# Performance work log

Hardware: AMD Instinct MI355X
Metric: run time of the kernel (lower is better)

## Reference

```python
import jax, jax.numpy as jnp
import numpy as np

IN_DIM = 768   # 256 + 256 + 128 + 128
OUT_DIM = 256
N_EDGES = 320000
N_GRAPHS = 64


def setup_inputs() -> dict:
    key = jax.random.key(0)
    ks = jax.random.split(key, 7)
    src = jax.random.normal(ks[0], (N_EDGES, 256), dtype=jnp.float32)
    dest = jax.random.normal(ks[1], (N_EDGES, 256), dtype=jnp.float32)
    edge_attr = jax.random.normal(ks[2], (N_EDGES, 128), dtype=jnp.float32)
    u = jax.random.normal(ks[3], (N_GRAPHS, 128), dtype=jnp.float32)
    batch = jnp.sort(jax.random.randint(ks[4], (N_EDGES,), 0, N_GRAPHS, dtype=jnp.int64)) if jax.config.read('jax_enable_x64') else jnp.sort(jax.random.randint(ks[4], (N_EDGES,), 0, N_GRAPHS)).astype(jnp.int32)
    # Linear(in_dim, out_dim): torch default init ~ U(-1/sqrt(in), 1/sqrt(in))
    bound = 1.0 / np.sqrt(IN_DIM)
    W = jax.random.uniform(ks[5], (IN_DIM, OUT_DIM), dtype=jnp.float32, minval=-bound, maxval=bound)
    b = jax.random.uniform(ks[6], (OUT_DIM,), dtype=jnp.float32, minval=-bound, maxval=bound)
    return {"src": src, "dest": dest, "edge_attr": edge_attr, "u": u, "batch": batch, "W": W, "b": b}


def reference(src, dest, edge_attr, u, batch, W, b):
    # u_expanded = u[batch]; concat [dest, src, edge_attr, u_exp]; Linear + ReLU
    u_exp = jnp.take(u, batch, axis=0)                    # [E, 128]
    combined = jnp.concatenate([dest, src, edge_attr, u_exp], axis=1)  # [E, 768]
    out = combined @ W + b                                # [E, 256]
    return jax.nn.relu(out)
```

## Files before the change

### kernel.cpp

```cpp
#include <hip/hip_runtime.h>
#include <cstdint>
#include <cstddef>

#define BM 64
#define BN 256
#define BK 32
#define NT 24
#define THREADS 512
#define A_BYTES (BM * BK * 2)
#define B_BYTES (BN * BK * 2)
#define BUF_BYTES (A_BYTES + B_BYTES)
#define NBUF 3

typedef __attribute__((ext_vector_type(4))) float f32x4;
typedef __attribute__((ext_vector_type(8))) short bf16x8;
typedef __attribute__((ext_vector_type(2))) unsigned int u32x2;

__device__ __forceinline__ unsigned int f2bf(float f) {
  union { float f; uint32_t u; } v; v.f = f;
  uint32_t r = v.u + 0x7FFFu + ((v.u >> 16) & 1u);
  return r >> 16;
}

__global__ void wt_kernel(const float* __restrict__ W, unsigned short* __restrict__ WtS) {
  const int gid = blockIdx.x * 256 + threadIdx.x;
  const int kt = gid >> 10;
  const int c  = gid & 1023;
  const int n  = ((c >> 6) << 4) | (c & 15);
  const int k0 = kt * 32 + ((c >> 4) & 3) * 8;
  unsigned int p[4];
#pragma unroll
  for (int i = 0; i < 4; ++i)
    p[i] = f2bf(W[(size_t)(k0 + 2 * i) * 256 + n]) |
           (f2bf(W[(size_t)(k0 + 2 * i + 1) * 256 + n]) << 16);
  *(u32x2*)((char*)WtS + (size_t)gid * 16)     = u32x2{p[0], p[1]};
  *(u32x2*)((char*)WtS + (size_t)gid * 16 + 8) = u32x2{p[2], p[3]};
}

__global__ __launch_bounds__(THREADS, 4) void edge_gemm(
    const float* __restrict__ srcf, const float* __restrict__ destf,
    const float* __restrict__ eaf, const float* __restrict__ uf,
    const int* __restrict__ batch, const unsigned short* __restrict__ WtS,
    const float* __restrict__ bias, float* __restrict__ out)
{
  __shared__ char smem[NBUF * BUF_BYTES];
  const int tid  = threadIdx.x;
  const int lane = tid & 63;
  const int w    = tid >> 6;
  const int wr   = w >> 2;
  const int wc   = w & 3;
  const int m0   = blockIdx.x * BM;
  const int l15  = lane & 15;
  const int l4   = lane >> 4;

  const int s_row  = ((tid >> 7) << 4) | ((tid >> 1) & 15);
  const int s_coff = (((tid >> 5) & 3) << 3) | ((tid & 1) << 2);
  const int s_ae   = m0 + s_row;
  const int s_ub   = batch[s_ae];

  float bs[4];
#pragma unroll
  for (int nf = 0; nf < 4; ++nf) bs[nf] = bias[wc * 64 + nf * 16 + l15];

  f32x4 acc[2][4];
  f32x4 z = {0.f, 0.f, 0.f, 0.f};
#pragma unroll
  for (int i = 0; i < 2; ++i)
#pragma unroll
    for (int j = 0; j < 4; ++j) acc[i][j] = z;

  auto a_ptr = [&](int kt) -> const float* {
    if (kt < 8)  return destf + (size_t)s_ae * 256 + kt * 32 + s_coff;
    if (kt < 16) return srcf  + (size_t)s_ae * 256 + (kt - 8) * 32 + s_coff;
    if (kt < 20) return eaf   + (size_t)s_ae * 128 + (kt - 16) * 32 + s_coff;
    return uf + (size_t)s_ub * 128 + (kt - 20) * 32 + s_coff;
  };

  f32x4 va[2];

  auto stage = [&](int kt) {
    char* Bb = smem + (kt % NBUF) * BUF_BYTES + A_BYTES;
    const char* wb = (const char*)WtS + (size_t)kt * B_BYTES;
#pragma unroll
    for (int j = 0; j < 2; ++j) {
      const char* g = wb + (size_t)(j * 512 + tid) * 16;
      char* l = Bb + (size_t)(j * 512 + w * 64) * 16;
      __builtin_amdgcn_global_load_lds(
          (const __attribute__((address_space(1))) uint32_t*)g,
          (__attribute__((address_space(3))) uint32_t*)l, 16, 0, 0);
    }
    va[kt & 1] = *(const f32x4*)a_ptr(kt);
  };
  auto write_a = [&](int kt) {
    char* Ab = smem + (kt % NBUF) * BUF_BYTES;
    f32x4 v = va[kt & 1];
    u32x2 p;
    p[0] = f2bf(v[0]) | (f2bf(v[1]) << 16);
    p[1] = f2bf(v[2]) | (f2bf(v[3]) << 16);
    *(u32x2*)(Ab + tid * 8) = p;
  };
  auto compute = [&](int kt) {
    const char* Ab = smem + (kt % NBUF) * BUF_BYTES;
    const char* Bb = Ab + A_BYTES;
    bf16x8 af[2], bfr[4];
#pragma unroll
    for (int mf = 0; mf < 2; ++mf)
      af[mf] = *(const bf16x8*)(Ab + (((wr * 2 + mf) * 64) + l4 * 16 + l15) * 16);
#pragma unroll
    for (int nf = 0; nf < 4; ++nf)
      bfr[nf] = *(const bf16x8*)(Bb + (((wc * 4 + nf) * 64) + l4 * 16 + l15) * 16);
#pragma unroll
    for (int mf = 0; mf < 2; ++mf)
#pragma unroll
      for (int nf = 0; nf < 4; ++nf)
        acc[mf][nf] = __builtin_amdgcn_mfma_f32_16x16x32_bf16(
            af[mf], bfr[nf], acc[mf][nf], 0, 0, 0);
  };

#define STEP_SYNC()                                          \
  asm volatile("s_waitcnt vmcnt(3)" ::: "memory");           \
  __builtin_amdgcn_sched_barrier(0);                         \
  asm volatile("s_waitcnt lgkmcnt(0)" ::: "memory");         \
  __builtin_amdgcn_sched_barrier(0);                         \
  __builtin_amdgcn_s_barrier()

  stage(0);
  __builtin_amdgcn_sched_barrier(0);
  stage(1);
  __builtin_amdgcn_sched_barrier(0);
  write_a(0);
  STEP_SYNC();

#pragma unroll
  for (int kt = 0; kt < NT; ++kt) {
    if (kt + 2 < NT) stage(kt + 2);
    __builtin_amdgcn_sched_barrier(0);
    compute(kt);
    if (kt + 1 < NT) {
      write_a(kt + 1);
      STEP_SYNC();
    }
  }

#pragma unroll
  for (int mf = 0; mf < 2; ++mf) {
    const int r0 = m0 + wr * 32 + mf * 16 + l4 * 4;
#pragma unroll
    for (int nf = 0; nf < 4; ++nf) {
      const int cn = wc * 64 + nf * 16 + l15;
      const f32x4 v = acc[mf][nf];
#pragma unroll
      for (int j = 0; j < 4; ++j) {
        const float x = v[j] + bs[nf];
        out[(size_t)(r0 + j) * 256 + cn] = x > 0.f ? x : 0.f;
      }
    }
  }
#undef STEP_SYNC
}

extern "C" void kernel_launch(void* const* d_in, const int* in_sizes, int n_in,
                              void* d_out, int out_size, void* d_ws, size_t ws_size,
                              hipStream_t stream) {
  const float* srcf  = (const float*)d_in[0];
  const float* destf = (const float*)d_in[1];
  const float* eaf   = (const float*)d_in[2];
  const float* uf    = (const float*)d_in[3];
  const int*   batch = (const int*)d_in[4];
  const float* W     = (const float*)d_in[5];
  const float* bias  = (const float*)d_in[6];
  float* out = (float*)d_out;
  unsigned short* WtS = (unsigned short*)d_ws;

  wt_kernel<<<96, 256, 0, stream>>>(W, WtS);

  edge_gemm<<<320000 / BM, THREADS, 0, stream>>>(
      srcf, destf, eaf, uf, batch, WtS, bias, out);
}
```

Baseline: 282.0 us.

## Stage A in 256-wide swizzled LDS slabs and read W directly from global

Replaces the per-32-K-step pipeline, which staged A and W tiles through LDS with a barrier every step, by three large stages of 256 K columns each. Every stage loads a full 64x256 A slab as coalesced row-wise loads into double-buffered, XOR-swizzled LDS, so the kernel needs only three barriers. The bf16 W fragments are now loaded straight from global or L2 into registers each step instead of going through LDS. This removes most synchronisation and W traffic through LDS, but adds per-step global loads for W with no latency hiding and uses more registers (eight f32x4 prefetch registers).

```diff
diff --git a/kernel.cpp b/kernel.cpp
--- a/kernel.cpp
+++ b/kernel.cpp
@@ -3,14 +3,9 @@
 #include <cstddef>
 
 #define BM 64
-#define BN 256
-#define BK 32
+#define THREADS 512
+#define A_SLAB 32768
 #define NT 24
-#define THREADS 512
-#define A_BYTES (BM * BK * 2)
-#define B_BYTES (BN * BK * 2)
-#define BUF_BYTES (A_BYTES + B_BYTES)
-#define NBUF 3
 
 typedef __attribute__((ext_vector_type(4))) float f32x4;
 typedef __attribute__((ext_vector_type(8))) short bf16x8;
@@ -43,7 +38,7 @@
     const int* __restrict__ batch, const unsigned short* __restrict__ WtS,
     const float* __restrict__ bias, float* __restrict__ out)
 {
-  __shared__ char smem[NBUF * BUF_BYTES];
+  __shared__ char smem[2 * A_SLAB];
   const int tid  = threadIdx.x;
   const int lane = tid & 63;
   const int w    = tid >> 6;
@@ -52,11 +47,11 @@
   const int m0   = blockIdx.x * BM;
   const int l15  = lane & 15;
   const int l4   = lane >> 4;
+  const int sw8  = w * 8;
 
-  const int s_row  = ((tid >> 7) << 4) | ((tid >> 1) & 15);
-  const int s_coff = (((tid >> 5) & 3) << 3) | ((tid & 1) << 2);
-  const int s_ae   = m0 + s_row;
-  const int s_ub   = batch[s_ae];
+  int ubi[4];
+#pragma unroll
+  for (int i = 0; i < 4; ++i) ubi[i] = batch[m0 + sw8 + 2 * i + (lane >> 5)];
 
   float bs[4];
 #pragma unroll
@@ -69,46 +64,68 @@
 #pragma unroll
     for (int j = 0; j < 4; ++j) acc[i][j] = z;
 
-  auto a_ptr = [&](int kt) -> const float* {
-    if (kt < 8)  return destf + (size_t)s_ae * 256 + kt * 32 + s_coff;
-    if (kt < 16) return srcf  + (size_t)s_ae * 256 + (kt - 8) * 32 + s_coff;
-    if (kt < 20) return eaf   + (size_t)s_ae * 128 + (kt - 16) * 32 + s_coff;
-    return uf + (size_t)s_ub * 128 + (kt - 20) * 32 + s_coff;
+  f32x4 sv[8];
+
+  auto issue_stage = [&](int ss) {
+    if (ss < 2) {
+      const float* base = (ss == 0) ? destf : srcf;
+#pragma unroll
+      for (int i = 0; i < 8; ++i)
+        sv[i] = *(const f32x4*)(base + (size_t)(m0 + sw8 + i) * 256 + lane * 4);
+    } else {
+#pragma unroll
+      for (int i = 0; i < 4; ++i)
+        sv[i] = *(const f32x4*)(eaf + (size_t)(m0 + sw8 + 2 * i + (lane >> 5)) * 128
+                                + (lane & 31) * 4);
+#pragma unroll
+      for (int i = 0; i < 4; ++i)
+        sv[4 + i] = *(const f32x4*)(uf + (size_t)ubi[i] * 128 + (lane & 31) * 4);
+    }
   };
 
-  f32x4 va[2];
-
-  auto stage = [&](int kt) {
-    char* Bb = smem + (kt % NBUF) * BUF_BYTES + A_BYTES;
-    const char* wb = (const char*)WtS + (size_t)kt * B_BYTES;
-#pragma unroll
-    for (int j = 0; j < 2; ++j) {
-      const char* g = wb + (size_t)(j * 512 + tid) * 16;
-      char* l = Bb + (size_t)(j * 512 + w * 64) * 16;
-      __builtin_amdgcn_global_load_lds(
-          (const __attribute__((address_space(1))) uint32_t*)g,
-          (__attribute__((address_space(3))) uint32_t*)l, 16, 0, 0);
-    }
-    va[kt & 1] = *(const f32x4*)a_ptr(kt);
-  };
-  auto write_a = [&](int kt) {
-    char* Ab = smem + (kt % NBUF) * BUF_BYTES;
-    f32x4 v = va[kt & 1];
+  auto cvt4 = [&](f32x4 v) -> u32x2 {
     u32x2 p;
     p[0] = f2bf(v[0]) | (f2bf(v[1]) << 16);
     p[1] = f2bf(v[2]) | (f2bf(v[3]) << 16);
-    *(u32x2*)(Ab + tid * 8) = p;
+    return p;
   };
-  auto compute = [&](int kt) {
-    const char* Ab = smem + (kt % NBUF) * BUF_BYTES;
-    const char* Bb = Ab + A_BYTES;
-    bf16x8 af[2], bfr[4];
+
+  auto write_slab = [&](int buf, int ss) {
+    char* Ab = smem + buf * A_SLAB;
+    if (ss < 2) {
 #pragma unroll
-    for (int mf = 0; mf < 2; ++mf)
-      af[mf] = *(const bf16x8*)(Ab + (((wr * 2 + mf) * 64) + l4 * 16 + l15) * 16);
+      for (int i = 0; i < 8; ++i) {
+        const int r = sw8 + i, c = lane >> 1;
+        *(u32x2*)(Ab + r * 512 + (((c ^ (r & 7)) << 4) | ((lane & 1) << 3))) = cvt4(sv[i]);
+      }
+    } else {
+#pragma unroll
+      for (int i = 0; i < 4; ++i) {
+        const int r = sw8 + 2 * i + (lane >> 5), c = (lane & 31) >> 1;
+        *(u32x2*)(Ab + r * 512 + (((c ^ (r & 7)) << 4) | ((lane & 1) << 3))) = cvt4(sv[i]);
+      }
+#pragma unroll
+      for (int i = 0; i < 4; ++i) {
+        const int r = sw8 + 2 * i + (lane >> 5), c = 16 + ((lane & 31) >> 1);
+        *(u32x2*)(Ab + r * 512 + (((c ^ (r & 7)) << 4) | ((lane & 1) << 3))) = cvt4(sv[4 + i]);
+      }
+    }
+  };
+
+  auto compute = [&](int buf, int kt) {
+    const char* Ab = smem + buf * A_SLAB;
+    const char* wb = (const char*)WtS + (size_t)kt * 16384;
+    bf16x8 bfr[4], af[2];
 #pragma unroll
     for (int nf = 0; nf < 4; ++nf)
-      bfr[nf] = *(const bf16x8*)(Bb + (((wc * 4 + nf) * 64) + l4 * 16 + l15) * 16);
+      bfr[nf] = *(const bf16x8*)(wb + (size_t)(((wc * 4 + nf) * 64 + l4 * 16 + l15)) * 16);
+    const int s = kt & 7;
+#pragma unroll
+    for (int mf = 0; mf < 2; ++mf) {
+      const int r = wr * 32 + mf * 16 + l15;
+      const int c = s * 4 + l4;
+      af[mf] = *(const bf16x8*)(Ab + r * 512 + ((c ^ (r & 7)) << 4));
+    }
 #pragma unroll
     for (int mf = 0; mf < 2; ++mf)
 #pragma unroll
@@ -117,28 +134,18 @@
             af[mf], bfr[nf], acc[mf][nf], 0, 0, 0);
   };
 
-#define STEP_SYNC()                                          \
-  asm volatile("s_waitcnt vmcnt(3)" ::: "memory");           \
-  __builtin_amdgcn_sched_barrier(0);                         \
-  asm volatile("s_waitcnt lgkmcnt(0)" ::: "memory");         \
-  __builtin_amdgcn_sched_barrier(0);                         \
-  __builtin_amdgcn_s_barrier()
-
-  stage(0);
-  __builtin_amdgcn_sched_barrier(0);
-  stage(1);
-  __builtin_amdgcn_sched_barrier(0);
-  write_a(0);
-  STEP_SYNC();
+  issue_stage(0);
+  write_slab(0, 0);
+  __syncthreads();
 
 #pragma unroll
-  for (int kt = 0; kt < NT; ++kt) {
-    if (kt + 2 < NT) stage(kt + 2);
-    __builtin_amdgcn_sched_barrier(0);
-    compute(kt);
-    if (kt + 1 < NT) {
-      write_a(kt + 1);
-      STEP_SYNC();
+  for (int ss = 0; ss < 3; ++ss) {
+    if (ss < 2) issue_stage(ss + 1);
+#pragma unroll
+    for (int s = 0; s < 8; ++s) compute(ss & 1, ss * 8 + s);
+    if (ss < 2) {
+      write_slab((ss + 1) & 1, ss + 1);
+      __syncthreads();
     }
   }
 
@@ -156,7 +163,6 @@
       }
     }
   }
-#undef STEP_SYNC
 }
 
 extern "C" void kernel_launch(void* const* d_in, const int* in_sizes, int n_in,
```

Measured after the change: 312.8 us. 10.9% more time.

## Switch to double-buffered pipeline with plain syncthreads and higher occupancy

Applied to the files above, without the earlier changes.

Replaces the triple-buffered, prefetch-distance-two pipeline with manual vmcnt/lgkmcnt waits by a double-buffered, prefetch-distance-one loop that uses __syncthreads each step. The launch bound is raised from 4 to 6 waves per SIMD, which frees LDS and registers so more blocks can be resident. The trade is less latency hiding per block, since global loads now have only one compute step to land and the full barrier waits on all outstanding memory ops, in exchange for more concurrent blocks.

```diff
diff --git a/kernel.cpp b/kernel.cpp
--- a/kernel.cpp
+++ b/kernel.cpp
@@ -10,7 +10,7 @@
 #define A_BYTES (BM * BK * 2)
 #define B_BYTES (BN * BK * 2)
 #define BUF_BYTES (A_BYTES + B_BYTES)
-#define NBUF 3
+#define NBUF 2
 
 typedef __attribute__((ext_vector_type(4))) float f32x4;
 typedef __attribute__((ext_vector_type(8))) short bf16x8;
@@ -37,7 +37,7 @@
   *(u32x2*)((char*)WtS + (size_t)gid * 16 + 8) = u32x2{p[2], p[3]};
 }
 
-__global__ __launch_bounds__(THREADS, 4) void edge_gemm(
+__global__ __launch_bounds__(THREADS, 6) void edge_gemm(
     const float* __restrict__ srcf, const float* __restrict__ destf,
     const float* __restrict__ eaf, const float* __restrict__ uf,
     const int* __restrict__ batch, const unsigned short* __restrict__ WtS,
@@ -76,10 +76,10 @@
     return uf + (size_t)s_ub * 128 + (kt - 20) * 32 + s_coff;
   };
 
-  f32x4 va[2];
+  f32x4 va;
 
   auto stage = [&](int kt) {
-    char* Bb = smem + (kt % NBUF) * BUF_BYTES + A_BYTES;
+    char* Bb = smem + (kt & 1) * BUF_BYTES + A_BYTES;
     const char* wb = (const char*)WtS + (size_t)kt * B_BYTES;
 #pragma unroll
     for (int j = 0; j < 2; ++j) {
@@ -89,18 +89,17 @@
           (const __attribute__((address_space(1))) uint32_t*)g,
           (__attribute__((address_space(3))) uint32_t*)l, 16, 0, 0);
     }
-    va[kt & 1] = *(const f32x4*)a_ptr(kt);
+    va = *(const f32x4*)a_ptr(kt);
   };
   auto write_a = [&](int kt) {
-    char* Ab = smem + (kt % NBUF) * BUF_BYTES;
-    f32x4 v = va[kt & 1];
+    char* Ab = smem + (kt & 1) * BUF_BYTES;
     u32x2 p;
-    p[0] = f2bf(v[0]) | (f2bf(v[1]) << 16);
-    p[1] = f2bf(v[2]) | (f2bf(v[3]) << 16);
+    p[0] = f2bf(va[0]) | (f2bf(va[1]) << 16);
+    p[1] = f2bf(va[2]) | (f2bf(va[3]) << 16);
     *(u32x2*)(Ab + tid * 8) = p;
   };
   auto compute = [&](int kt) {
-    const char* Ab = smem + (kt % NBUF) * BUF_BYTES;
+    const char* Ab = smem + (kt & 1) * BUF_BYTES;
     const char* Bb = Ab + A_BYTES;
     bf16x8 af[2], bfr[4];
 #pragma unroll
@@ -117,29 +116,16 @@
             af[mf], bfr[nf], acc[mf][nf], 0, 0, 0);
   };
 
-#define STEP_SYNC()                                          \
-  asm volatile("s_waitcnt vmcnt(3)" ::: "memory");           \
-  __builtin_amdgcn_sched_barrier(0);                         \
-  asm volatile("s_waitcnt lgkmcnt(0)" ::: "memory");         \
-  __builtin_amdgcn_sched_barrier(0);                         \
-  __builtin_amdgcn_s_barrier()
-
   stage(0);
-  __builtin_amdgcn_sched_barrier(0);
-  stage(1);
-  __builtin_amdgcn_sched_barrier(0);
   write_a(0);
-  STEP_SYNC();
+  __syncthreads();
 
 #pragma unroll
   for (int kt = 0; kt < NT; ++kt) {
-    if (kt + 2 < NT) stage(kt + 2);
-    __builtin_amdgcn_sched_barrier(0);
+    if (kt + 1 < NT) stage(kt + 1);
     compute(kt);
-    if (kt + 1 < NT) {
-      write_a(kt + 1);
-      STEP_SYNC();
-    }
+    if (kt + 1 < NT) write_a(kt + 1);
+    __syncthreads();
   }
 
 #pragma unroll
@@ -156,7 +142,6 @@
       }
     }
   }
-#undef STEP_SYNC
 }
 
 extern "C" void kernel_launch(void* const* d_in, const int* in_sizes, int n_in,
```

Result: slower. 302.7 us (+7.4%).
